# Performance work log

Hardware: AMD Instinct MI355X
Metric: run time of the kernel (lower is better)

The kernel has to match this reference:

```python
import jax, jax.numpy as jnp
import numpy as np

# Config matching init_kwargs
D_MODEL = 1024   # input_size
D_HEAD = 2048    # head_size (expert hidden)
N_EXPERTS = 8
TOP_K = 2


def setup_inputs() -> dict:
    key = jax.random.key(0)
    k_x, k_g, k_w1, k_b1, k_w2, k_b2 = jax.random.split(key, 6)
    B, S = 4, 1024
    x = jax.random.normal(k_x, (B, S, D_MODEL), dtype=jnp.float32)
    # f_gate: nn.Linear(input_size, num_experts, bias=False) -> weight [E, D]
    gate_w = jax.random.normal(k_g, (N_EXPERTS, D_MODEL), dtype=jnp.float32) * 0.02
    # experts: ParallelExperts weights [E, in, out]
    s1 = 1.0 / D_MODEL
    s2 = 1.0 / D_HEAD
    w1 = jax.random.uniform(k_w1, (N_EXPERTS, D_MODEL, D_HEAD), jnp.float32, -s1, s1)
    b1 = jax.random.uniform(k_b1, (N_EXPERTS, D_HEAD), jnp.float32, -s1, s1)
    w2 = jax.random.uniform(k_w2, (N_EXPERTS, D_HEAD, D_MODEL), jnp.float32, -s2, s2)
    b2 = jax.random.uniform(k_b2, (N_EXPERTS, D_MODEL), jnp.float32, -s2, s2)
    return {"x": x, "gate_w": gate_w, "w1": w1, "b1": b1, "w2": w2, "b2": b2}


def reference(x, gate_w, w1, b1, w2, b2):
    B, S, D = x.shape
    xt = x.reshape(-1, D)                                   # [N, D]
    N = xt.shape[0]
    # --- gating (noisy_gating=False, eval path of top_k_gating) ---
    logits = xt @ gate_w.T                                  # [N, E]
    probs = jax.nn.softmax(logits, axis=-1)
    top_g, top_i = jax.lax.top_k(probs, TOP_K)              # [N, k]
    # gates = zeros.scatter(1, top_k_indices, top_k_gates)
    gates = jnp.zeros_like(probs).at[jnp.arange(N)[:, None], top_i].set(top_g)  # [N, E]
    # --- dispatch / grouped GEMM / combine ---
    # Equivalent dense-per-expert form: gates[n,e]==0 for non-routed tokens,
    # so y[n] = sum_e gates[n,e] * f_e(x[n]) exactly matches the
    # sort/scatter + per-expert torch.mm dispatch of ParallelLinear.
    y = jnp.zeros_like(xt)
    for e in range(N_EXPERTS):
        h = jax.nn.gelu(xt @ w1[e] + b1[e], approximate=False)  # [N, H]
        y = y + gates[:, e:e + 1] * (h @ w2[e] + b2[e])
    return y.reshape(B, S, D)
```

## Files before the change

### kernel.cpp

```cpp
#include <hip/hip_runtime.h>
#include <hip/hip_bf16.h>
#include <cstdint>
#include <cstddef>

#define N_TOK 4096
#define DM    1024
#define DH    2048
#define NE    8
#define BM    128
#define BN    128
#define BK    64
#define MAXT  80
#define HROWS (MAXT * BM)

typedef unsigned short u16t;
typedef __attribute__((ext_vector_type(4))) float          f32x4;
typedef __attribute__((ext_vector_type(8))) unsigned short u16x8;

__device__ __forceinline__ u16t f2b(float f) {
  union { float f; unsigned u; } v; v.f = f;
  return (u16t)((v.u + 0x7FFFu + ((v.u >> 16) & 1u)) >> 16);
}

__device__ __forceinline__ void gload16(const void* g, void* l) {
  auto gp = (const __attribute__((address_space(1))) unsigned int*)(uintptr_t)g;
  auto lp = (__attribute__((address_space(3))) unsigned int*)(uintptr_t)l;
  __builtin_amdgcn_global_load_lds(gp, lp, 16, 0, 0);
}

__device__ __forceinline__ void mfma16(f32x4& c, u16x8 a, u16x8 b) {
  asm("v_mfma_f32_16x16x32_bf16 %0, %1, %2, %0" : "+v"(c) : "v"(a), "v"(b));
}

__global__ void k_cvt_x(const float* __restrict__ x, u16t* __restrict__ x16) {
  int i = blockIdx.x * blockDim.x + threadIdx.x;
  float4 v = reinterpret_cast<const float4*>(x)[i];
  ushort4 o;
  o.x = f2b(v.x); o.y = f2b(v.y); o.z = f2b(v.z); o.w = f2b(v.w);
  reinterpret_cast<ushort4*>(x16)[i] = o;
}

__global__ void k_tr_cvt(const float* __restrict__ src, u16t* __restrict__ dst, int R, int C) {
  __shared__ float t[64][65];
  const float* s = src + (size_t)blockIdx.z * R * C;
  u16t* d = dst + (size_t)blockIdx.z * R * C;
  int r0 = blockIdx.y * 64, c0 = blockIdx.x * 64;
#pragma unroll
  for (int i = 0; i < 16; ++i) {
    int idx = i * 256 + threadIdx.x;
    int r = idx >> 6, c = idx & 63;
    t[r][c] = s[(size_t)(r0 + r) * C + (c0 + c)];
  }
  __syncthreads();
#pragma unroll
  for (int i = 0; i < 16; ++i) {
    int idx = i * 256 + threadIdx.x;
    int rr = idx >> 6, cc = idx & 63;
    d[(size_t)(c0 + rr) * R + (r0 + cc)] = f2b(t[cc][rr]);
  }
}

__global__ void __launch_bounds__(256) k_gate(const float* __restrict__ x,
                                              const float* __restrict__ gw,
                                              int* __restrict__ topi,
                                              float* __restrict__ topg) {
  __shared__ float gws[NE * DM];
  int tid = threadIdx.x;
#pragma unroll
  for (int i = 0; i < NE * DM / 256; ++i) gws[i * 256 + tid] = gw[i * 256 + tid];
  __syncthreads();
  int wv = tid >> 6, lane = tid & 63;
  int t = blockIdx.x * 4 + wv;
  float acc[NE];
#pragma unroll
  for (int e = 0; e < NE; ++e) acc[e] = 0.f;
  const float* xr = x + (size_t)t * DM;
#pragma unroll
  for (int c = 0; c < DM / 64; ++c) {
    float xv = xr[c * 64 + lane];
#pragma unroll
    for (int e = 0; e < NE; ++e) acc[e] += xv * gws[e * DM + c * 64 + lane];
  }
#pragma unroll
  for (int e = 0; e < NE; ++e) {
#pragma unroll
    for (int m = 1; m < 64; m <<= 1) acc[e] += __shfl_xor(acc[e], m);
  }
  float mx = acc[0];
#pragma unroll
  for (int e = 1; e < NE; ++e) mx = fmaxf(mx, acc[e]);
  float p[NE], s = 0.f;
#pragma unroll
  for (int e = 0; e < NE; ++e) { p[e] = expf(acc[e] - mx); s += p[e]; }
  float inv = 1.f / s;
#pragma unroll
  for (int e = 0; e < NE; ++e) p[e] *= inv;
  int i1 = 0; float g1 = p[0];
#pragma unroll
  for (int e = 1; e < NE; ++e) if (p[e] > g1) { g1 = p[e]; i1 = e; }
  int i2 = -1; float g2 = -1.f;
#pragma unroll
  for (int e = 0; e < NE; ++e) if (e != i1 && p[e] > g2) { g2 = p[e]; i2 = e; }
  if (lane == 0) {
    topi[t * 2 + 0] = i1; topi[t * 2 + 1] = i2;
    topg[t * 2 + 0] = g1; topg[t * 2 + 1] = g2;
  }
}

__global__ void __launch_bounds__(1024) k_scan(const int* __restrict__ topi,
                                               int* __restrict__ offe,
                                               int* __restrict__ cur64,
                                               int* __restrict__ te,
                                               int* __restrict__ trs,
                                               int* __restrict__ tnr,
                                               int* __restrict__ ntiles) {
  __shared__ int hist[NE];
  int tid = threadIdx.x;
  if (tid < NE) { hist[tid] = 0; cur64[tid * 16] = 0; }
  __syncthreads();
  int lc[NE];
#pragma unroll
  for (int e = 0; e < NE; ++e) lc[e] = 0;
#pragma unroll
  for (int i = 0; i < (N_TOK * 2) / 1024; ++i) {
    int v = topi[tid * ((N_TOK * 2) / 1024) + i];
#pragma unroll
    for (int e = 0; e < NE; ++e) lc[e] += (v == e);
  }
#pragma unroll
  for (int e = 0; e < NE; ++e) {
#pragma unroll
    for (int m = 1; m < 64; m <<= 1) lc[e] += __shfl_xor(lc[e], m);
  }
  if ((tid & 63) == 0) {
#pragma unroll
    for (int e = 0; e < NE; ++e) atomicAdd(&hist[e], lc[e]);
  }
  __syncthreads();
  if (tid == 0) {
    int off = 0, nt = 0;
    for (int e = 0; e < NE; ++e) {
      offe[e] = off;
      int c = hist[e];
      for (int i = 0; i < c; i += BM) {
        te[nt] = e; trs[nt] = off + i; tnr[nt] = min(BM, c - i); ++nt;
      }
      off += c;
    }
    *ntiles = nt;
  }
}

__global__ void k_scatter(const int* __restrict__ topi, const int* __restrict__ offe,
                          int* __restrict__ cur64, int* __restrict__ pair) {
  int t = blockIdx.x * blockDim.x + threadIdx.x;
  int lane = threadIdx.x & 63;
#pragma unroll
  for (int s = 0; s < 2; ++s) {
    int e = topi[t * 2 + s];
    int pos = 0;
#pragma unroll
    for (int ee = 0; ee < NE; ++ee) {
      unsigned long long mask = __ballot(e == ee);
      if (e == ee) {
        int rank = __popcll(mask & ((1ull << lane) - 1ull));
        int leader = __ffsll((long long)mask) - 1;
        int base = 0;
        if (lane == leader) base = atomicAdd(&cur64[ee * 16], (int)__popcll(mask));
        base = __shfl(base, leader);
        pos = offe[ee] + base + rank;
      }
    }
    pair[pos] = t * 2 + s;
  }
}

__global__ void __launch_bounds__(256, 2) k_gemm1(
    const u16t* __restrict__ x16, const u16t* __restrict__ w1t,
    const float* __restrict__ b1, u16t* __restrict__ h16,
    const int* __restrict__ pair, const int* __restrict__ te,
    const int* __restrict__ trs, const int* __restrict__ tnr,
    const int* __restrict__ ntiles) {
  int ty = blockIdx.y;
  if (ty >= *ntiles) return;
  int e = te[ty], rs = trs[ty], nr = tnr[ty];
  int n0 = blockIdx.x * BN;
  __shared__ u16t As[2][BM * BK];
  __shared__ u16t Bs[2][BN * BK];
  __shared__ int tok[BM];
  int tid = threadIdx.x;
  if (tid < BM) {
    int r = tid;
    int p = rs + (r < nr ? r : nr - 1);
    tok[r] = pair[p] >> 1;
  }
  __syncthreads();
  const u16t* aptr[4]; const u16t* bptr[4];
#pragma unroll
  for (int it = 0; it < 4; ++it) {
    int idx = it * 256 + tid;
    int r = idx >> 3, c = idx & 7;
    int cs = c ^ (r & 7);
    aptr[it] = x16 + (size_t)tok[r] * DM + cs * 8;
    bptr[it] = w1t + (size_t)e * DH * DM + (size_t)(n0 + r) * DM + cs * 8;
  }
  f32x4 acc[4][4];
#pragma unroll
  for (int m = 0; m < 4; ++m)
#pragma unroll
    for (int n = 0; n < 4; ++n) acc[m][n] = {0.f, 0.f, 0.f, 0.f};
  int lane = tid & 63, wv = tid >> 6;
  int wr = (wv >> 1) * 64, wc = (wv & 1) * 64;
#pragma unroll
  for (int it = 0; it < 4; ++it) {
    int idx = it * 256 + tid;
    gload16(aptr[it], &As[0][idx * 8]);
    gload16(bptr[it], &Bs[0][idx * 8]);
  }
  __syncthreads();
  const int NK = DM / BK;
  for (int ks = 0; ks < NK; ++ks) {
    int cur = ks & 1;
    if (ks + 1 < NK) {
      int k1 = (ks + 1) * BK;
#pragma unroll
      for (int it = 0; it < 4; ++it) {
        int idx = it * 256 + tid;
        gload16(aptr[it] + k1, &As[cur ^ 1][idx * 8]);
        gload16(bptr[it] + k1, &Bs[cur ^ 1][idx * 8]);
      }
    }
#pragma unroll
    for (int kk = 0; kk < 2; ++kk) {
      u16x8 af[4], bf[4];
#pragma unroll
      for (int m = 0; m < 4; ++m) {
        int row = wr + m * 16 + (lane & 15);
        int cs = (kk * 4 + (lane >> 4)) ^ (row & 7);
        af[m] = *reinterpret_cast<const u16x8*>(&As[cur][row * BK + cs * 8]);
      }
#pragma unroll
      for (int n = 0; n < 4; ++n) {
        int row = wc + n * 16 + (lane & 15);
        int cs = (kk * 4 + (lane >> 4)) ^ (row & 7);
        bf[n] = *reinterpret_cast<const u16x8*>(&Bs[cur][row * BK + cs * 8]);
      }
#pragma unroll
      for (int m = 0; m < 4; ++m)
#pragma unroll
        for (int n = 0; n < 4; ++n) mfma16(acc[m][n], af[m], bf[n]);
    }
    __syncthreads();
  }
#pragma unroll
  for (int n = 0; n < 4; ++n) {
    int col = n0 + wc + n * 16 + (lane & 15);
    float bias = b1[e * DH + col];
#pragma unroll
    for (int m = 0; m < 4; ++m) {
#pragma unroll
      for (int r = 0; r < 4; ++r) {
        int rl = wr + m * 16 + ((lane >> 4) << 2) + r;
        if (rl < nr) {
          float z = acc[m][n][r] + bias;
          float g = 0.5f * z * (1.0f + erff(z * 0.70710678118654752440f));
          h16[(size_t)(rs + rl) * DH + col] = f2b(g);
        }
      }
    }
  }
}

__global__ void __launch_bounds__(256, 2) k_gemm2(
    const u16t* __restrict__ h16, const u16t* __restrict__ w2t,
    const float* __restrict__ b2, float* __restrict__ out,
    const int* __restrict__ pair, const float* __restrict__ topg,
    const int* __restrict__ te, const int* __restrict__ trs,
    const int* __restrict__ tnr, const int* __restrict__ ntiles) {
  int ty = blockIdx.y;
  if (ty >= *ntiles) return;
  int e = te[ty], rs = trs[ty], nr = tnr[ty];
  int n0 = blockIdx.x * BN;
  __shared__ u16t As[2][BM * BK];
  __shared__ u16t Bs[2][BN * BK];
  __shared__ int tsl[BM];
  __shared__ float gl[BM];
  int tid = threadIdx.x;
  if (tid < BM) {
    int r = tid;
    int p = rs + (r < nr ? r : nr - 1);
    int ts = pair[p];
    tsl[r] = ts;
    gl[r] = topg[ts];
  }
  __syncthreads();
  const u16t* aptr[4]; const u16t* bptr[4];
#pragma unroll
  for (int it = 0; it < 4; ++it) {
    int idx = it * 256 + tid;
    int r = idx >> 3, c = idx & 7;
    int cs = c ^ (r & 7);
    aptr[it] = h16 + (size_t)(rs + r) * DH + cs * 8;
    bptr[it] = w2t + (size_t)e * DM * DH + (size_t)(n0 + r) * DH + cs * 8;
  }
  f32x4 acc[4][4];
#pragma unroll
  for (int m = 0; m < 4; ++m)
#pragma unroll
    for (int n = 0; n < 4; ++n) acc[m][n] = {0.f, 0.f, 0.f, 0.f};
  int lane = tid & 63, wv = tid >> 6;
  int wr = (wv >> 1) * 64, wc = (wv & 1) * 64;
#pragma unroll
  for (int it = 0; it < 4; ++it) {
    int idx = it * 256 + tid;
    gload16(aptr[it], &As[0][idx * 8]);
    gload16(bptr[it], &Bs[0][idx * 8]);
  }
  __syncthreads();
  const int NK = DH / BK;
  for (int ks = 0; ks < NK; ++ks) {
    int cur = ks & 1;
    if (ks + 1 < NK) {
      int k1 = (ks + 1) * BK;
#pragma unroll
      for (int it = 0; it < 4; ++it) {
        int idx = it * 256 + tid;
        gload16(aptr[it] + k1, &As[cur ^ 1][idx * 8]);
        gload16(bptr[it] + k1, &Bs[cur ^ 1][idx * 8]);
      }
    }
#pragma unroll
    for (int kk = 0; kk < 2; ++kk) {
      u16x8 af[4], bf[4];
#pragma unroll
      for (int m = 0; m < 4; ++m) {
        int row = wr + m * 16 + (lane & 15);
        int cs = (kk * 4 + (lane >> 4)) ^ (row & 7);
        af[m] = *reinterpret_cast<const u16x8*>(&As[cur][row * BK + cs * 8]);
      }
#pragma unroll
      for (int n = 0; n < 4; ++n) {
        int row = wc + n * 16 + (lane & 15);
        int cs = (kk * 4 + (lane >> 4)) ^ (row & 7);
        bf[n] = *reinterpret_cast<const u16x8*>(&Bs[cur][row * BK + cs * 8]);
      }
#pragma unroll
      for (int m = 0; m < 4; ++m)
#pragma unroll
        for (int n = 0; n < 4; ++n) mfma16(acc[m][n], af[m], bf[n]);
    }
    __syncthreads();
  }
  float bias[4];
#pragma unroll
  for (int n = 0; n < 4; ++n) bias[n] = b2[e * DM + n0 + wc + n * 16 + (lane & 15)];
#pragma unroll
  for (int m = 0; m < 4; ++m) {
#pragma unroll
    for (int r = 0; r < 4; ++r) {
      int rl = wr + m * 16 + ((lane >> 4) << 2) + r;
      if (rl < nr) {
        int ts = tsl[rl];
        float g = gl[rl];
        float* orow = out + (size_t)(ts >> 1) * DM;
#pragma unroll
        for (int n = 0; n < 4; ++n) {
          int col = n0 + wc + n * 16 + (lane & 15);
          float v = g * (acc[m][n][r] + bias[n]);
          unsafeAtomicAdd(&orow[col], v);
        }
      }
    }
  }
}

extern "C" void kernel_launch(void* const* d_in, const int* in_sizes, int n_in,
                              void* d_out, int out_size, void* d_ws, size_t ws_size,
                              hipStream_t stream) {
  const float* x  = (const float*)d_in[0];
  const float* gw = (const float*)d_in[1];
  const float* w1 = (const float*)d_in[2];
  const float* b1 = (const float*)d_in[3];
  const float* w2 = (const float*)d_in[4];
  const float* b2 = (const float*)d_in[5];
  float* out = (float*)d_out;
  char* ws = (char*)d_ws;

  size_t o = 0;
  auto alloc = [&](size_t b) { size_t p = o; o += (b + 255) & ~(size_t)255; return p; };
  size_t X16  = alloc((size_t)N_TOK * DM * 2);
  size_t W1T  = alloc((size_t)NE * DH * DM * 2);
  size_t W2T  = alloc((size_t)NE * DM * DH * 2);
  size_t HB   = alloc((size_t)HROWS * DH * 2);
  size_t TOPI = alloc((size_t)N_TOK * 2 * 4);
  size_t TOPG = alloc((size_t)N_TOK * 2 * 4);
  size_t PAIR = alloc((size_t)HROWS * 4);
  size_t CUR  = alloc(NE * 64);
  size_t OFE  = alloc(64);
  size_t TE   = alloc(MAXT * 4);
  size_t TRS  = alloc(MAXT * 4);
  size_t TNR  = alloc(MAXT * 4);
  size_t NT   = alloc(64);
  (void)ws_size; (void)in_sizes; (void)n_in;

  hipMemsetAsync(out, 0, (size_t)out_size * 4, stream);

  k_cvt_x<<<N_TOK * DM / 1024, 256, 0, stream>>>(x, (u16t*)(ws + X16));
  k_tr_cvt<<<dim3(DH / 64, DM / 64, NE), 256, 0, stream>>>(w1, (u16t*)(ws + W1T), DM, DH);
  k_tr_cvt<<<dim3(DM / 64, DH / 64, NE), 256, 0, stream>>>(w2, (u16t*)(ws + W2T), DH, DM);
  k_gate<<<N_TOK / 4, 256, 0, stream>>>(x, gw, (int*)(ws + TOPI), (float*)(ws + TOPG));
  k_scan<<<1, 1024, 0, stream>>>((int*)(ws + TOPI), (int*)(ws + OFE), (int*)(ws + CUR),
                                 (int*)(ws + TE), (int*)(ws + TRS), (int*)(ws + TNR),
                                 (int*)(ws + NT));
  k_scatter<<<N_TOK / 256, 256, 0, stream>>>((int*)(ws + TOPI), (int*)(ws + OFE),
                                             (int*)(ws + CUR), (int*)(ws + PAIR));
  k_gemm1<<<dim3(DH / BN, MAXT), 256, 0, stream>>>(
      (const u16t*)(ws + X16), (const u16t*)(ws + W1T), b1, (u16t*)(ws + HB),
      (const int*)(ws + PAIR), (const int*)(ws + TE), (const int*)(ws + TRS),
      (const int*)(ws + TNR), (const int*)(ws + NT));
  k_gemm2<<<dim3(DM / BN, MAXT), 256, 0, stream>>>(
      (const u16t*)(ws + HB), (const u16t*)(ws + W2T), b2, out,
      (const int*)(ws + PAIR), (const float*)(ws + TOPG), (const int*)(ws + TE),
      (const int*)(ws + TRS), (const int*)(ws + TNR), (const int*)(ws + NT));
}
```

Measured before the change: 245.0 us.

## Enlarge MoE expert GEMM tiles to 256 rows with 512-thread blocks

Grows the per-expert row tile from 128 to 256 tokens and both GEMM kernels to 512 threads (8 waves). GEMM1 now uses 256x256 tiles with each wave holding a 128x64 accumulator, and GEMM2 uses 256x128 tiles. A-fragment loads are interleaved with the MFMA loop. The aim is more reuse of each loaded weight tile and fewer tile launches. The cost is more wasted rows in partial per-expert tiles, fewer blocks to fill the GPU, and higher register and LDS use at one block per CU.

```diff
diff --git a/kernel.cpp b/kernel.cpp
--- a/kernel.cpp
+++ b/kernel.cpp
@@ -7,11 +7,12 @@
 #define DM    1024
 #define DH    2048
 #define NE    8
-#define BM    128
-#define BN    128
+#define TBM   256
+#define BN1   256
+#define BN2   128
 #define BK    64
-#define MAXT  80
-#define HROWS (MAXT * BM)
+#define MAXT  40
+#define HROWS (MAXT * TBM)
 
 typedef unsigned short u16t;
 typedef __attribute__((ext_vector_type(4))) float          f32x4;
@@ -142,8 +143,8 @@
     for (int e = 0; e < NE; ++e) {
       offe[e] = off;
       int c = hist[e];
-      for (int i = 0; i < c; i += BM) {
-        te[nt] = e; trs[nt] = off + i; tnr[nt] = min(BM, c - i); ++nt;
+      for (int i = 0; i < c; i += TBM) {
+        te[nt] = e; trs[nt] = off + i; tnr[nt] = min(TBM, c - i); ++nt;
       }
       off += c;
     }
@@ -175,7 +176,7 @@
   }
 }
 
-__global__ void __launch_bounds__(256, 2) k_gemm1(
+__global__ void __launch_bounds__(512, 1) k_gemm1(
     const u16t* __restrict__ x16, const u16t* __restrict__ w1t,
     const float* __restrict__ b1, u16t* __restrict__ h16,
     const int* __restrict__ pair, const int* __restrict__ te,
@@ -184,36 +185,36 @@
   int ty = blockIdx.y;
   if (ty >= *ntiles) return;
   int e = te[ty], rs = trs[ty], nr = tnr[ty];
-  int n0 = blockIdx.x * BN;
-  __shared__ u16t As[2][BM * BK];
-  __shared__ u16t Bs[2][BN * BK];
-  __shared__ int tok[BM];
+  int n0 = blockIdx.x * BN1;
+  __shared__ u16t As[2][TBM * BK];
+  __shared__ u16t Bs[2][BN1 * BK];
+  __shared__ int tok[TBM];
   int tid = threadIdx.x;
-  if (tid < BM) {
-    int r = tid;
-    int p = rs + (r < nr ? r : nr - 1);
-    tok[r] = pair[p] >> 1;
+  if (tid < TBM) {
+    int p = rs + (tid < nr ? tid : nr - 1);
+    tok[tid] = pair[p] >> 1;
   }
   __syncthreads();
   const u16t* aptr[4]; const u16t* bptr[4];
 #pragma unroll
   for (int it = 0; it < 4; ++it) {
-    int idx = it * 256 + tid;
+    int idx = it * 512 + tid;
     int r = idx >> 3, c = idx & 7;
     int cs = c ^ (r & 7);
     aptr[it] = x16 + (size_t)tok[r] * DM + cs * 8;
     bptr[it] = w1t + (size_t)e * DH * DM + (size_t)(n0 + r) * DM + cs * 8;
   }
-  f32x4 acc[4][4];
-#pragma unroll
-  for (int m = 0; m < 4; ++m)
+  f32x4 acc[8][4];
+#pragma unroll
+  for (int m = 0; m < 8; ++m)
 #pragma unroll
     for (int n = 0; n < 4; ++n) acc[m][n] = {0.f, 0.f, 0.f, 0.f};
   int lane = tid & 63, wv = tid >> 6;
-  int wr = (wv >> 1) * 64, wc = (wv & 1) * 64;
+  int wm = wv >> 2, wn = wv & 3;
+  int wrO = wm * 128, wcO = wn * 64;
 #pragma unroll
   for (int it = 0; it < 4; ++it) {
-    int idx = it * 256 + tid;
+    int idx = it * 512 + tid;
     gload16(aptr[it], &As[0][idx * 8]);
     gload16(bptr[it], &Bs[0][idx * 8]);
   }
@@ -225,42 +226,40 @@
       int k1 = (ks + 1) * BK;
 #pragma unroll
       for (int it = 0; it < 4; ++it) {
-        int idx = it * 256 + tid;
+        int idx = it * 512 + tid;
         gload16(aptr[it] + k1, &As[cur ^ 1][idx * 8]);
         gload16(bptr[it] + k1, &Bs[cur ^ 1][idx * 8]);
       }
     }
 #pragma unroll
     for (int kk = 0; kk < 2; ++kk) {
-      u16x8 af[4], bf[4];
-#pragma unroll
-      for (int m = 0; m < 4; ++m) {
-        int row = wr + m * 16 + (lane & 15);
-        int cs = (kk * 4 + (lane >> 4)) ^ (row & 7);
-        af[m] = *reinterpret_cast<const u16x8*>(&As[cur][row * BK + cs * 8]);
-      }
+      u16x8 bf[4];
 #pragma unroll
       for (int n = 0; n < 4; ++n) {
-        int row = wc + n * 16 + (lane & 15);
+        int row = wcO + n * 16 + (lane & 15);
         int cs = (kk * 4 + (lane >> 4)) ^ (row & 7);
         bf[n] = *reinterpret_cast<const u16x8*>(&Bs[cur][row * BK + cs * 8]);
       }
 #pragma unroll
-      for (int m = 0; m < 4; ++m)
-#pragma unroll
-        for (int n = 0; n < 4; ++n) mfma16(acc[m][n], af[m], bf[n]);
+      for (int m = 0; m < 8; ++m) {
+        int row = wrO + m * 16 + (lane & 15);
+        int cs = (kk * 4 + (lane >> 4)) ^ (row & 7);
+        u16x8 af = *reinterpret_cast<const u16x8*>(&As[cur][row * BK + cs * 8]);
+#pragma unroll
+        for (int n = 0; n < 4; ++n) mfma16(acc[m][n], af, bf[n]);
+      }
     }
     __syncthreads();
   }
 #pragma unroll
   for (int n = 0; n < 4; ++n) {
-    int col = n0 + wc + n * 16 + (lane & 15);
+    int col = n0 + wcO + n * 16 + (lane & 15);
     float bias = b1[e * DH + col];
 #pragma unroll
-    for (int m = 0; m < 4; ++m) {
+    for (int m = 0; m < 8; ++m) {
 #pragma unroll
       for (int r = 0; r < 4; ++r) {
-        int rl = wr + m * 16 + ((lane >> 4) << 2) + r;
+        int rl = wrO + m * 16 + ((lane >> 4) << 2) + r;
         if (rl < nr) {
           float z = acc[m][n][r] + bias;
           float g = 0.5f * z * (1.0f + erff(z * 0.70710678118654752440f));
@@ -271,7 +270,7 @@
   }
 }
 
-__global__ void __launch_bounds__(256, 2) k_gemm2(
+__global__ void __launch_bounds__(512, 1) k_gemm2(
     const u16t* __restrict__ h16, const u16t* __restrict__ w2t,
     const float* __restrict__ b2, float* __restrict__ out,
     const int* __restrict__ pair, const float* __restrict__ topg,
@@ -280,27 +279,32 @@
   int ty = blockIdx.y;
   if (ty >= *ntiles) return;
   int e = te[ty], rs = trs[ty], nr = tnr[ty];
-  int n0 = blockIdx.x * BN;
-  __shared__ u16t As[2][BM * BK];
-  __shared__ u16t Bs[2][BN * BK];
-  __shared__ int tsl[BM];
-  __shared__ float gl[BM];
+  int n0 = blockIdx.x * BN2;
+  __shared__ u16t As[2][TBM * BK];
+  __shared__ u16t Bs[2][BN2 * BK];
+  __shared__ int tsl[TBM];
+  __shared__ float gl[TBM];
   int tid = threadIdx.x;
-  if (tid < BM) {
-    int r = tid;
-    int p = rs + (r < nr ? r : nr - 1);
+  if (tid < TBM) {
+    int p = rs + (tid < nr ? tid : nr - 1);
     int ts = pair[p];
-    tsl[r] = ts;
-    gl[r] = topg[ts];
-  }
-  __syncthreads();
-  const u16t* aptr[4]; const u16t* bptr[4];
+    tsl[tid] = ts;
+    gl[tid] = topg[ts];
+  }
+  __syncthreads();
+  const u16t* aptr[4]; const u16t* bptr[2];
 #pragma unroll
   for (int it = 0; it < 4; ++it) {
-    int idx = it * 256 + tid;
+    int idx = it * 512 + tid;
     int r = idx >> 3, c = idx & 7;
     int cs = c ^ (r & 7);
     aptr[it] = h16 + (size_t)(rs + r) * DH + cs * 8;
+  }
+#pragma unroll
+  for (int it = 0; it < 2; ++it) {
+    int idx = it * 512 + tid;
+    int r = idx >> 3, c = idx & 7;
+    int cs = c ^ (r & 7);
     bptr[it] = w2t + (size_t)e * DM * DH + (size_t)(n0 + r) * DH + cs * 8;
   }
   f32x4 acc[4][4];
@@ -309,11 +313,16 @@
 #pragma unroll
     for (int n = 0; n < 4; ++n) acc[m][n] = {0.f, 0.f, 0.f, 0.f};
   int lane = tid & 63, wv = tid >> 6;
-  int wr = (wv >> 1) * 64, wc = (wv & 1) * 64;
+  int wm = wv >> 1, wn = wv & 1;
+  int wrO = wm * 64, wcO = wn * 64;
 #pragma unroll
   for (int it = 0; it < 4; ++it) {
-    int idx = it * 256 + tid;
+    int idx = it * 512 + tid;
     gload16(aptr[it], &As[0][idx * 8]);
+  }
+#pragma unroll
+  for (int it = 0; it < 2; ++it) {
+    int idx = it * 512 + tid;
     gload16(bptr[it], &Bs[0][idx * 8]);
   }
   __syncthreads();
@@ -324,48 +333,50 @@
       int k1 = (ks + 1) * BK;
 #pragma unroll
       for (int it = 0; it < 4; ++it) {
-        int idx = it * 256 + tid;
+        int idx = it * 512 + tid;
         gload16(aptr[it] + k1, &As[cur ^ 1][idx * 8]);
+      }
+#pragma unroll
+      for (int it = 0; it < 2; ++it) {
+        int idx = it * 512 + tid;
         gload16(bptr[it] + k1, &Bs[cur ^ 1][idx * 8]);
       }
     }
 #pragma unroll
     for (int kk = 0; kk < 2; ++kk) {
-      u16x8 af[4], bf[4];
-#pragma unroll
-      for (int m = 0; m < 4; ++m) {
-        int row = wr + m * 16 + (lane & 15);
-        int cs = (kk * 4 + (lane >> 4)) ^ (row & 7);
-        af[m] = *reinterpret_cast<const u16x8*>(&As[cur][row * BK + cs * 8]);
-      }
+      u16x8 bf[4];
 #pragma unroll
       for (int n = 0; n < 4; ++n) {
-        int row = wc + n * 16 + (lane & 15);
+        int row = wcO + n * 16 + (lane & 15);
         int cs = (kk * 4 + (lane >> 4)) ^ (row & 7);
         bf[n] = *reinterpret_cast<const u16x8*>(&Bs[cur][row * BK + cs * 8]);
       }
 #pragma unroll
-      for (int m = 0; m < 4; ++m)
-#pragma unroll
-        for (int n = 0; n < 4; ++n) mfma16(acc[m][n], af[m], bf[n]);
+      for (int m = 0; m < 4; ++m) {
+        int row = wrO + m * 16 + (lane & 15);
+        int cs = (kk * 4 + (lane >> 4)) ^ (row & 7);
+        u16x8 af = *reinterpret_cast<const u16x8*>(&As[cur][row * BK + cs * 8]);
+#pragma unroll
+        for (int n = 0; n < 4; ++n) mfma16(acc[m][n], af, bf[n]);
+      }
     }
     __syncthreads();
   }
   float bias[4];
 #pragma unroll
-  for (int n = 0; n < 4; ++n) bias[n] = b2[e * DM + n0 + wc + n * 16 + (lane & 15)];
+  for (int n = 0; n < 4; ++n) bias[n] = b2[e * DM + n0 + wcO + n * 16 + (lane & 15)];
 #pragma unroll
   for (int m = 0; m < 4; ++m) {
 #pragma unroll
     for (int r = 0; r < 4; ++r) {
-      int rl = wr + m * 16 + ((lane >> 4) << 2) + r;
+      int rl = wrO + m * 16 + ((lane >> 4) << 2) + r;
       if (rl < nr) {
         int ts = tsl[rl];
         float g = gl[rl];
         float* orow = out + (size_t)(ts >> 1) * DM;
 #pragma unroll
         for (int n = 0; n < 4; ++n) {
-          int col = n0 + wc + n * 16 + (lane & 15);
+          int col = n0 + wcO + n * 16 + (lane & 15);
           float v = g * (acc[m][n][r] + bias[n]);
           unsafeAtomicAdd(&orow[col], v);
         }
@@ -414,11 +425,11 @@
                                  (int*)(ws + NT));
   k_scatter<<<N_TOK / 256, 256, 0, stream>>>((int*)(ws + TOPI), (int*)(ws + OFE),
                                              (int*)(ws + CUR), (int*)(ws + PAIR));
-  k_gemm1<<<dim3(DH / BN, MAXT), 256, 0, stream>>>(
+  k_gemm1<<<dim3(DH / BN1, MAXT), 512, 0, stream>>>(
       (const u16t*)(ws + X16), (const u16t*)(ws + W1T), b1, (u16t*)(ws + HB),
       (const int*)(ws + PAIR), (const int*)(ws + TE), (const int*)(ws + TRS),
       (const int*)(ws + TNR), (const int*)(ws + NT));
-  k_gemm2<<<dim3(DM / BN, MAXT), 256, 0, stream>>>(
+  k_gemm2<<<dim3(DM / BN2, MAXT), 512, 0, stream>>>(
       (const u16t*)(ws + HB), (const u16t*)(ws + W2T), b2, out,
       (const int*)(ws + PAIR), (const float*)(ws + TOPG), (const int*)(ws + TE),
       (const int*)(ws + TRS), (const int*)(ws + TNR), (const int*)(ws + NT));
```

Measured after the change: 269.7 us. 1.1x slower.
